# Kernel tuning notes

Measured on AMD Instinct MI355X. Metric: run time of the kernel, lower is better.

The kernel has to match this reference:

```python
import jax, jax.numpy as jnp
import numpy as np

D = 256  # atom_feature_dim
LN_EPS = 1e-5
NEG_SLOPE = 0.01  # LeakyReLU default


def setup_inputs() -> dict:
    key = jax.random.key(0)
    ks = jax.random.split(key, 8)
    B, N, L = 16, 256, 1024
    inv = 1.0 / np.sqrt(D)
    return {
        "mol_atom_feature": jax.random.normal(ks[0], (B, N, D), jnp.float32),
        "atom_feature": jax.random.normal(ks[1], (B, L, D), jnp.float32),
        "mol_atom_attend_mask": jnp.ones((B, L), jnp.float32),
        "mol_atom_softmax_mask": jnp.zeros((B, L), jnp.float32),
        # nn.Linear(D, D) params (weight stored [out, in] torch-style; we use x @ W.T form via einsum)
        "W_mol": jax.random.uniform(ks[2], (D, D), jnp.float32, -inv, inv),
        "b_mol": jnp.zeros((D,), jnp.float32),
        "W_nb": jax.random.uniform(ks[3], (D, D), jnp.float32, -inv, inv),
        "b_nb": jnp.zeros((D,), jnp.float32),
        # nn.Linear(2D, 1): weight [2D], bias scalar
        "align_w": jax.random.uniform(ks[4], (2 * D,), jnp.float32, -1.0 / np.sqrt(2 * D), 1.0 / np.sqrt(2 * D)),
        "align_b": jnp.zeros((), jnp.float32),
        "ln_gamma": jnp.ones((D,), jnp.float32),
        "ln_beta": jnp.zeros((D,), jnp.float32),
    }


def reference(mol_atom_feature, atom_feature, mol_atom_attend_mask, mol_atom_softmax_mask,
              W_mol, b_mol, W_nb, b_nb, align_w, align_b, ln_gamma, ln_beta):
    # Linear transforms (dropout is identity in eval)
    x = jnp.einsum('bnd,ed->bne', mol_atom_feature, W_mol) + b_mol   # [B,N,D]
    a = jnp.einsum('bld,ed->ble', atom_feature, W_nb) + b_nb        # [B,L,D]

    # GAT align: Linear over concat([x_i, a_j]) is separable:
    # score[b,n,l] = x[b,n]@w1 + a[b,l]@w2 + b
    w1, w2 = align_w[:D], align_w[D:]
    score = (x @ w1)[:, :, None] + (a @ w2)[:, None, :] + align_b   # [B,N,L]
    score = jax.nn.leaky_relu(score, NEG_SLOPE)

    # additive softmax mask over atom axis, then masked softmax + attend mask
    score = score + mol_atom_softmax_mask[:, None, :]
    attn = jax.nn.softmax(score, axis=-1)
    attn = attn * mol_atom_attend_mask[:, None, :]

    # weighted aggregation of transformed atom features
    ctx = jnp.einsum('bnl,bld->bnd', attn, a)                        # [B,N,D]

    # LayerNorm
    mu = jnp.mean(ctx, axis=-1, keepdims=True)
    var = jnp.var(ctx, axis=-1, keepdims=True)
    out = (ctx - mu) * jax.lax.rsqrt(var + LN_EPS) * ln_gamma + ln_beta
    return out
```

## Files before the change

kernel.cpp:

```cpp
#include <hip/hip_runtime.h>
#include <hip/hip_bf16.h>
#include <math.h>

#define BB 16
#define NN 256
#define LL 1024
#define DD 256

constexpr float LN_EPS = 1e-5f;
constexpr float NEG_SLOPE = 0.01f;

typedef __attribute__((ext_vector_type(8))) short short8;
typedef __attribute__((ext_vector_type(4))) float f32x4;
typedef __attribute__((ext_vector_type(4))) int i32x4;

static __device__ __forceinline__ unsigned cvtpk(float lo, float hi) {
  __hip_bfloat162 h = __float22bfloat162_rn(make_float2(lo, hi));
  union { __hip_bfloat162 h; unsigned u; } v; v.h = h;
  return v.u;
}
static __device__ __forceinline__ short8 pack8(float4 f0, float4 f1) {
  union { i32x4 i; short8 s; } v;
  v.i.x = cvtpk(f0.x, f0.y);
  v.i.y = cvtpk(f0.z, f0.w);
  v.i.z = cvtpk(f1.x, f1.y);
  v.i.w = cvtpk(f1.z, f1.w);
  return v.s;
}
static __device__ __forceinline__ unsigned short f2bf(float f) {
  union { float f; unsigned u; } v; v.f = f;
  unsigned r = v.u + 0x7FFFu + ((v.u >> 16) & 1u);
  return (unsigned short)(r >> 16);
}

__global__ __launch_bounds__(512) void agemm_kernel(
    const float* __restrict__ atom, const float* __restrict__ W_nb,
    const float* __restrict__ b_nb, const float* __restrict__ W_mol,
    const float* __restrict__ b_mol, const float* __restrict__ align_w,
    const float* __restrict__ align_b, unsigned short* __restrict__ aT,
    float* __restrict__ s2g, float* __restrict__ v1c) {
  __shared__ char atile[64 * 256 * 2];
  __shared__ unsigned short sAT[256 * 68];
  __shared__ float vp[32][16];
  __shared__ float s2p[8][66];

  int t = threadIdx.x;
  int w = t >> 6, lane = t & 63;
  int i = blockIdx.x;
  int x = i & 7, k = i >> 3;
  int b = x + 8 * (k >> 4);
  int l0 = (k & 15) * 64;
  int lo16 = lane & 15, g = lane >> 4;

  {
    int r = t >> 3, dseg = (t & 7) * 32;
    const float* src = atom + (size_t)(b * LL + l0 + r) * DD + dseg;
    #pragma unroll
    for (int q = 0; q < 4; ++q) {
      float4 f0 = *(const float4*)(src + q * 8);
      float4 f1 = *(const float4*)(src + q * 8 + 4);
      int byte = ((r * 256 + dseg + q * 8) * 2) ^ ((r & 7) << 4);
      *(short8*)(atile + byte) = pack8(f0, f1);
    }
  }

  if (i < 16) {
    int d0 = i * 16;
    int dl = t & 15, eseg = t >> 4;
    float acc = 0.f;
    #pragma unroll
    for (int q = 0; q < 8; ++q) {
      int e = eseg * 8 + q;
      acc += align_w[e] * W_mol[e * DD + d0 + dl];
    }
    vp[eseg][dl] = acc;
    __syncthreads();
    if (t < 16) {
      float s = 0.f;
      #pragma unroll
      for (int q = 0; q < 32; ++q) s += vp[q][t];
      v1c[d0 + t] = s;
    }
    if (i == 0 && w == 1) {
      float s = b_mol[lane] * align_w[lane] +
                b_mol[lane + 64] * align_w[lane + 64] +
                b_mol[lane + 128] * align_w[lane + 128] +
                b_mol[lane + 192] * align_w[lane + 192];
      #pragma unroll
      for (int off = 32; off > 0; off >>= 1) s += __shfl_xor(s, off, 64);
      if (lane == 0) v1c[256] = s + align_b[0];
    }
  }
  __syncthreads();

  f32x4 acc[2][4];
  #pragma unroll
  for (int m = 0; m < 2; ++m)
    #pragma unroll
    for (int n = 0; n < 4; ++n) acc[m][n] = f32x4{0.f, 0.f, 0.f, 0.f};

  const float* Ap = W_nb + (size_t)(w * 32 + lo16) * DD + g * 8;

  #pragma unroll 2
  for (int kk = 0; kk < 8; ++kk) {
    short8 af[2];
    #pragma unroll
    for (int m = 0; m < 2; ++m) {
      float4 f0 = *(const float4*)(Ap + m * 16 * DD + kk * 32);
      float4 f1 = *(const float4*)(Ap + m * 16 * DD + kk * 32 + 4);
      af[m] = pack8(f0, f1);
    }
    short8 bf[4];
    #pragma unroll
    for (int n = 0; n < 4; ++n) {
      int l = n * 16 + lo16;
      int byte = ((l * 256 + kk * 32 + g * 8) * 2) ^ ((l & 7) << 4);
      bf[n] = *(const short8*)(atile + byte);
    }
    #pragma unroll
    for (int m = 0; m < 2; ++m)
      #pragma unroll
      for (int n = 0; n < 4; ++n)
        acc[m][n] = __builtin_amdgcn_mfma_f32_16x16x32_bf16(af[m], bf[n],
                                                            acc[m][n], 0, 0, 0);
  }

  {
    float4 bias[2], w2r[2];
    #pragma unroll
    for (int m = 0; m < 2; ++m) {
      bias[m] = *(const float4*)&b_nb[w * 32 + m * 16 + g * 4];
      w2r[m] = *(const float4*)&align_w[DD + w * 32 + m * 16 + g * 4];
    }
    float p[4] = {0.f, 0.f, 0.f, 0.f};
    #pragma unroll
    for (int m = 0; m < 2; ++m) {
      #pragma unroll
      for (int n = 0; n < 4; ++n) {
        int l = n * 16 + lo16;
        #pragma unroll
        for (int jj = 0; jj < 4; ++jj) {
          float v = acc[m][n][jj] + ((const float*)&bias[m])[jj];
          sAT[(w * 32 + m * 16 + g * 4 + jj) * 68 + l] = f2bf(v);
          p[n] += ((const float*)&w2r[m])[jj] * v;
        }
      }
    }
    #pragma unroll
    for (int n = 0; n < 4; ++n) {
      p[n] += __shfl_xor(p[n], 16, 64);
      p[n] += __shfl_xor(p[n], 32, 64);
    }
    if (g == 0) {
      #pragma unroll
      for (int n = 0; n < 4; ++n) s2p[w][n * 16 + lo16] = p[n];
    }
  }
  __syncthreads();

  if (t < 64) {
    float s = 0.f;
    #pragma unroll
    for (int q = 0; q < 8; ++q) s += s2p[q][t];
    s2g[b * LL + l0 + t] = s;
  }
  unsigned short* dst = aT + (size_t)b * DD * LL + l0;
  #pragma unroll
  for (int idx = t; idx < 4096; idx += 512) {
    int e = idx >> 4, ch = idx & 15;
    ushort4 v = *(const ushort4*)&sAT[e * 68 + ch * 4];
    *(ushort4*)(dst + (size_t)e * LL + ch * 4) = v;
  }
}

__global__ __launch_bounds__(512) void attn_kernel(
    const unsigned short* __restrict__ aT, const float* __restrict__ mol,
    const float* __restrict__ v1c, const float* __restrict__ s2,
    const float* __restrict__ amask, const float* __restrict__ smask,
    const float* __restrict__ gamma, const float* __restrict__ beta,
    float* __restrict__ out) {
  __shared__ unsigned short sattn[16 * 1024];
  __shared__ float ctxp[2][16][DD];
  __shared__ float v1s[256];
  __shared__ float s1s[16];
  __shared__ float mu_s[16], rs_s[16];
  int i = blockIdx.x;
  int x = i & 7, k = i >> 3;
  int b = x + 8 * (k >> 4);
  int n0 = (k & 15) * 16;
  int t = threadIdx.x, w = t >> 6, lane = t & 63;

  float c0 = v1c[256];
  if (t < 256) v1s[t] = v1c[t];
  __syncthreads();

  {
    int r = t >> 5, off = (t & 31) * 8;
    const float* mr = mol + (size_t)(b * NN + n0 + r) * DD + off;
    float s = 0.f;
    #pragma unroll
    for (int q = 0; q < 2; ++q) {
      float4 f = *(const float4*)(mr + q * 4);
      s += f.x * v1s[off + q * 4] + f.y * v1s[off + q * 4 + 1] +
           f.z * v1s[off + q * 4 + 2] + f.w * v1s[off + q * 4 + 3];
    }
    s += __shfl_xor(s, 1, 64);
    s += __shfl_xor(s, 2, 64);
    s += __shfl_xor(s, 4, 64);
    s += __shfl_xor(s, 8, 64);
    s += __shfl_xor(s, 16, 64);
    if ((t & 31) == 0) s1s[r] = s + c0;
  }
  __syncthreads();

  {
    float s2v[16], amv[16], smv[16];
    #pragma unroll
    for (int q = 0; q < 16; ++q) {
      int l = lane + 64 * q;
      s2v[q] = s2[b * LL + l];
      amv[q] = amask[b * LL + l];
      smv[q] = smask[b * LL + l];
    }
    #pragma unroll
    for (int rr = 0; rr < 2; ++rr) {
      int r = w * 2 + rr;
      float s1v = s1s[r];
      float p[16];
      float mx = -INFINITY;
      #pragma unroll
      for (int q = 0; q < 16; ++q) {
        float sc = s1v + s2v[q];
        sc = sc > 0.f ? sc : NEG_SLOPE * sc;
        sc += smv[q];
        p[q] = sc;
        mx = fmaxf(mx, sc);
      }
      #pragma unroll
      for (int off = 32; off > 0; off >>= 1) mx = fmaxf(mx, __shfl_xor(mx, off, 64));
      float sum = 0.f;
      #pragma unroll
      for (int q = 0; q < 16; ++q) {
        p[q] = __expf(p[q] - mx);
        sum += p[q];
      }
      #pragma unroll
      for (int off = 32; off > 0; off >>= 1) sum += __shfl_xor(sum, off, 64);
      float inv = 1.f / sum;
      #pragma unroll
      for (int q = 0; q < 16; ++q) {
        unsigned short bv = f2bf(p[q] * amv[q] * inv);
        int l = lane + 64 * q;
        int byte = ((r * 1024 + l) * 2) ^ ((r & 7) << 4);
        *(unsigned short*)((char*)sattn + byte) = bv;
      }
    }
  }
  __syncthreads();

  int lo16 = lane & 15, g = lane >> 4;
  {
    int e0 = (w & 3) * 64, lh = w >> 2;
    f32x4 acc[4];
    #pragma unroll
    for (int n = 0; n < 4; ++n) acc[n] = f32x4{0.f, 0.f, 0.f, 0.f};
    const unsigned short* Bp =
        aT + (size_t)b * DD * LL + (size_t)(e0 + lo16) * LL + lh * 512 + g * 8;
    #pragma unroll 4
    for (int kk = 0; kk < 16; ++kk) {
      short8 afr = *(const short8*)((const char*)sattn +
          (((lo16 * 1024 + lh * 512 + kk * 32 + g * 8) * 2) ^ ((lo16 & 7) << 4)));
      #pragma unroll
      for (int n = 0; n < 4; ++n) {
        short8 bfr = *(const short8*)(Bp + (size_t)n * 16 * LL + kk * 32);
        acc[n] = __builtin_amdgcn_mfma_f32_16x16x32_bf16(afr, bfr, acc[n], 0, 0, 0);
      }
    }
    #pragma unroll
    for (int n = 0; n < 4; ++n)
      #pragma unroll
      for (int jj = 0; jj < 4; ++jj)
        ctxp[lh][g * 4 + jj][e0 + n * 16 + lo16] = acc[n][jj];
  }
  __syncthreads();

  #pragma unroll
  for (int rr = 0; rr < 2; ++rr) {
    int r = w * 2 + rr;
    float s = 0.f, sq = 0.f;
    #pragma unroll
    for (int jj = 0; jj < 4; ++jj) {
      int cc = lane + 64 * jj;
      float v = ctxp[0][r][cc] + ctxp[1][r][cc];
      s += v;
      sq += v * v;
    }
    #pragma unroll
    for (int off = 32; off > 0; off >>= 1) {
      s += __shfl_xor(s, off, 64);
      sq += __shfl_xor(sq, off, 64);
    }
    if (lane == 0) {
      float mu = s * (1.f / 256.f);
      float var = sq * (1.f / 256.f) - mu * mu;
      mu_s[r] = mu;
      rs_s[r] = rsqrtf(var + LN_EPS);
    }
  }
  __syncthreads();

  #pragma unroll
  for (int q = 0; q < 8; ++q) {
    int idx = t + 512 * q;
    int r = idx >> 8, d = idx & 255;
    float v = ctxp[0][r][d] + ctxp[1][r][d];
    out[(size_t)(b * NN + n0 + r) * DD + d] =
        (v - mu_s[r]) * rs_s[r] * gamma[d] + beta[d];
  }
}

extern "C" void kernel_launch(void* const* d_in, const int* in_sizes, int n_in,
                              void* d_out, int out_size, void* d_ws, size_t ws_size,
                              hipStream_t stream) {
  const float* mol     = (const float*)d_in[0];
  const float* atom    = (const float*)d_in[1];
  const float* amask   = (const float*)d_in[2];
  const float* smask   = (const float*)d_in[3];
  const float* W_mol   = (const float*)d_in[4];
  const float* b_mol   = (const float*)d_in[5];
  const float* W_nb    = (const float*)d_in[6];
  const float* b_nb    = (const float*)d_in[7];
  const float* align_w = (const float*)d_in[8];
  const float* align_b = (const float*)d_in[9];
  const float* gamma   = (const float*)d_in[10];
  const float* beta    = (const float*)d_in[11];
  float* outp = (float*)d_out;

  char* wsb = (char*)d_ws;
  unsigned short* aT = (unsigned short*)wsb;
  float* s2g = (float*)(wsb + 8388608);
  float* v1c = s2g + BB * LL;

  agemm_kernel<<<256, 512, 0, stream>>>(atom, W_nb, b_nb, W_mol, b_mol,
                                        align_w, align_b, aT, s2g, v1c);
  attn_kernel<<<256, 512, 0, stream>>>(aT, mol, v1c, s2g, amask, smask,
                                       gamma, beta, outp);
}
```

Baseline: 39.30 us.

## Fuse projection and attention kernels with per-batch atomic counter handoff

Merges the two launches into one 512-block grid. The first 256 blocks compute the atom projection and signal completion per batch through an atomic counter. The remaining blocks each recompute the W_mol·w1 vector locally and spin-wait on that counter before running the attention. This removes a kernel launch gap and lets mol-side work overlap the projection, at the cost of an extra memset, redundant v1 computation in every block, and a deadlock risk if consumer blocks become resident before all producers. Shared memory is unioned across the two phases so that more blocks can be resident at once.

```diff
diff --git a/kernel.cpp b/kernel.cpp
--- a/kernel.cpp
+++ b/kernel.cpp
@@ -33,289 +33,294 @@
   return (unsigned short)(r >> 16);
 }
 
-__global__ __launch_bounds__(512) void agemm_kernel(
-    const float* __restrict__ atom, const float* __restrict__ W_nb,
-    const float* __restrict__ b_nb, const float* __restrict__ W_mol,
-    const float* __restrict__ b_mol, const float* __restrict__ align_w,
-    const float* __restrict__ align_b, unsigned short* __restrict__ aT,
-    float* __restrict__ s2g, float* __restrict__ v1c) {
-  __shared__ char atile[64 * 256 * 2];
-  __shared__ unsigned short sAT[256 * 68];
-  __shared__ float vp[32][16];
-  __shared__ float s2p[8][66];
-
-  int t = threadIdx.x;
-  int w = t >> 6, lane = t & 63;
-  int i = blockIdx.x;
-  int x = i & 7, k = i >> 3;
-  int b = x + 8 * (k >> 4);
-  int l0 = (k & 15) * 64;
+struct P1 {
+  char atile[64 * 256 * 2];
+  unsigned short sAT[256 * 68];
+  float s2p[8][66];
+};
+struct P2 {
+  unsigned short sattn[16 * 1024];
+  float ctxp[2][16][DD];
+  float vp2[2][256];
+};
+
+__global__ __launch_bounds__(512, 4) void fused_kernel(
+    const float* __restrict__ mol, const float* __restrict__ atom,
+    const float* __restrict__ amask, const float* __restrict__ smask,
+    const float* __restrict__ W_mol, const float* __restrict__ b_mol,
+    const float* __restrict__ W_nb, const float* __restrict__ b_nb,
+    const float* __restrict__ align_w, const float* __restrict__ align_b,
+    const float* __restrict__ gamma, const float* __restrict__ beta,
+    unsigned short* __restrict__ aT, float* __restrict__ s2g,
+    unsigned int* __restrict__ cnt, float* __restrict__ out) {
+  __shared__ union { P1 p1; P2 p2; } sh;
+  __shared__ float v1s[256];
+  __shared__ float s1s[16], mu_s[16], rs_s[16];
+  __shared__ float c0s;
+
+  int t = threadIdx.x, w = t >> 6, lane = t & 63;
   int lo16 = lane & 15, g = lane >> 4;
 
-  {
-    int r = t >> 3, dseg = (t & 7) * 32;
-    const float* src = atom + (size_t)(b * LL + l0 + r) * DD + dseg;
+  if (blockIdx.x < 256) {
+    int i = blockIdx.x;
+    int x = i & 7, k = i >> 3;
+    int b = x + 8 * (k >> 4);
+    int l0 = (k & 15) * 64;
+
+    {
+      int r = t >> 3, dseg = (t & 7) * 32;
+      const float* src = atom + (size_t)(b * LL + l0 + r) * DD + dseg;
+      #pragma unroll
+      for (int q = 0; q < 4; ++q) {
+        float4 f0 = *(const float4*)(src + q * 8);
+        float4 f1 = *(const float4*)(src + q * 8 + 4);
+        int byte = ((r * 256 + dseg + q * 8) * 2) ^ ((r & 7) << 4);
+        *(short8*)(sh.p1.atile + byte) = pack8(f0, f1);
+      }
+    }
+    __syncthreads();
+
+    f32x4 acc[2][4];
     #pragma unroll
-    for (int q = 0; q < 4; ++q) {
-      float4 f0 = *(const float4*)(src + q * 8);
-      float4 f1 = *(const float4*)(src + q * 8 + 4);
-      int byte = ((r * 256 + dseg + q * 8) * 2) ^ ((r & 7) << 4);
-      *(short8*)(atile + byte) = pack8(f0, f1);
-    }
-  }
-
-  if (i < 16) {
-    int d0 = i * 16;
-    int dl = t & 15, eseg = t >> 4;
-    float acc = 0.f;
+    for (int m = 0; m < 2; ++m)
+      #pragma unroll
+      for (int n = 0; n < 4; ++n) acc[m][n] = f32x4{0.f, 0.f, 0.f, 0.f};
+
+    const float* Ap = W_nb + (size_t)(w * 32 + lo16) * DD + g * 8;
+    #pragma unroll 2
+    for (int kk = 0; kk < 8; ++kk) {
+      short8 af[2];
+      #pragma unroll
+      for (int m = 0; m < 2; ++m) {
+        float4 f0 = *(const float4*)(Ap + m * 16 * DD + kk * 32);
+        float4 f1 = *(const float4*)(Ap + m * 16 * DD + kk * 32 + 4);
+        af[m] = pack8(f0, f1);
+      }
+      short8 bf[4];
+      #pragma unroll
+      for (int n = 0; n < 4; ++n) {
+        int l = n * 16 + lo16;
+        int byte = ((l * 256 + kk * 32 + g * 8) * 2) ^ ((l & 7) << 4);
+        bf[n] = *(const short8*)(sh.p1.atile + byte);
+      }
+      #pragma unroll
+      for (int m = 0; m < 2; ++m)
+        #pragma unroll
+        for (int n = 0; n < 4; ++n)
+          acc[m][n] = __builtin_amdgcn_mfma_f32_16x16x32_bf16(af[m], bf[n],
+                                                              acc[m][n], 0, 0, 0);
+    }
+
+    {
+      float4 bias[2], w2r[2];
+      #pragma unroll
+      for (int m = 0; m < 2; ++m) {
+        bias[m] = *(const float4*)&b_nb[w * 32 + m * 16 + g * 4];
+        w2r[m] = *(const float4*)&align_w[DD + w * 32 + m * 16 + g * 4];
+      }
+      float p[4] = {0.f, 0.f, 0.f, 0.f};
+      #pragma unroll
+      for (int m = 0; m < 2; ++m) {
+        #pragma unroll
+        for (int n = 0; n < 4; ++n) {
+          int l = n * 16 + lo16;
+          #pragma unroll
+          for (int jj = 0; jj < 4; ++jj) {
+            float v = acc[m][n][jj] + ((const float*)&bias[m])[jj];
+            sh.p1.sAT[(w * 32 + m * 16 + g * 4 + jj) * 68 + l] = f2bf(v);
+            p[n] += ((const float*)&w2r[m])[jj] * v;
+          }
+        }
+      }
+      #pragma unroll
+      for (int n = 0; n < 4; ++n) {
+        p[n] += __shfl_xor(p[n], 16, 64);
+        p[n] += __shfl_xor(p[n], 32, 64);
+      }
+      if (g == 0) {
+        #pragma unroll
+        for (int n = 0; n < 4; ++n) sh.p1.s2p[w][n * 16 + lo16] = p[n];
+      }
+    }
+    __syncthreads();
+
+    if (t < 64) {
+      float s = 0.f;
+      #pragma unroll
+      for (int q = 0; q < 8; ++q) s += sh.p1.s2p[q][t];
+      s2g[b * LL + l0 + t] = s;
+    }
+    unsigned short* dst = aT + (size_t)b * DD * LL + l0;
     #pragma unroll
-    for (int q = 0; q < 8; ++q) {
-      int e = eseg * 8 + q;
-      acc += align_w[e] * W_mol[e * DD + d0 + dl];
-    }
-    vp[eseg][dl] = acc;
-    __syncthreads();
-    if (t < 16) {
-      float s = 0.f;
-      #pragma unroll
-      for (int q = 0; q < 32; ++q) s += vp[q][t];
-      v1c[d0 + t] = s;
-    }
-    if (i == 0 && w == 1) {
+    for (int idx = t; idx < 4096; idx += 512) {
+      int e = idx >> 4, ch = idx & 15;
+      ushort4 v = *(const ushort4*)&sh.p1.sAT[e * 68 + ch * 4];
+      *(ushort4*)(dst + (size_t)e * LL + ch * 4) = v;
+    }
+    __syncthreads();
+
+    if (t == 0) {
+      __hip_atomic_fetch_add(&cnt[b], 1u, __ATOMIC_RELEASE,
+                             __HIP_MEMORY_SCOPE_AGENT);
+    }
+  } else {
+    int j = blockIdx.x - 256;
+    int x = j & 7, k = j >> 3;
+    int b = x + 8 * (k >> 4);
+    int n0 = (k & 15) * 16;
+
+    {
+      int d = t & 255, eh = t >> 8;
+      float acc = 0.f;
+      #pragma unroll 8
+      for (int e = eh * 128; e < eh * 128 + 128; ++e)
+        acc += align_w[e] * W_mol[e * DD + d];
+      sh.p2.vp2[eh][d] = acc;
+    }
+    if (w == 7) {
       float s = b_mol[lane] * align_w[lane] +
                 b_mol[lane + 64] * align_w[lane + 64] +
                 b_mol[lane + 128] * align_w[lane + 128] +
                 b_mol[lane + 192] * align_w[lane + 192];
       #pragma unroll
       for (int off = 32; off > 0; off >>= 1) s += __shfl_xor(s, off, 64);
-      if (lane == 0) v1c[256] = s + align_b[0];
-    }
-  }
-  __syncthreads();
-
-  f32x4 acc[2][4];
-  #pragma unroll
-  for (int m = 0; m < 2; ++m)
-    #pragma unroll
-    for (int n = 0; n < 4; ++n) acc[m][n] = f32x4{0.f, 0.f, 0.f, 0.f};
-
-  const float* Ap = W_nb + (size_t)(w * 32 + lo16) * DD + g * 8;
-
-  #pragma unroll 2
-  for (int kk = 0; kk < 8; ++kk) {
-    short8 af[2];
-    #pragma unroll
-    for (int m = 0; m < 2; ++m) {
-      float4 f0 = *(const float4*)(Ap + m * 16 * DD + kk * 32);
-      float4 f1 = *(const float4*)(Ap + m * 16 * DD + kk * 32 + 4);
-      af[m] = pack8(f0, f1);
-    }
-    short8 bf[4];
-    #pragma unroll
-    for (int n = 0; n < 4; ++n) {
-      int l = n * 16 + lo16;
-      int byte = ((l * 256 + kk * 32 + g * 8) * 2) ^ ((l & 7) << 4);
-      bf[n] = *(const short8*)(atile + byte);
-    }
-    #pragma unroll
-    for (int m = 0; m < 2; ++m)
+      if (lane == 0) c0s = s + align_b[0];
+    }
+    __syncthreads();
+    if (t < 256) v1s[t] = sh.p2.vp2[0][t] + sh.p2.vp2[1][t];
+    __syncthreads();
+
+    {
+      int r = t >> 5, off = (t & 31) * 8;
+      const float* mr = mol + (size_t)(b * NN + n0 + r) * DD + off;
+      float s = 0.f;
+      #pragma unroll
+      for (int q = 0; q < 2; ++q) {
+        float4 f = *(const float4*)(mr + q * 4);
+        s += f.x * v1s[off + q * 4] + f.y * v1s[off + q * 4 + 1] +
+             f.z * v1s[off + q * 4 + 2] + f.w * v1s[off + q * 4 + 3];
+      }
+      s += __shfl_xor(s, 1, 64);
+      s += __shfl_xor(s, 2, 64);
+      s += __shfl_xor(s, 4, 64);
+      s += __shfl_xor(s, 8, 64);
+      s += __shfl_xor(s, 16, 64);
+      if ((t & 31) == 0) s1s[r] = s + c0s;
+    }
+    __syncthreads();
+
+    if (t == 0) {
+      while (__hip_atomic_load(&cnt[b], __ATOMIC_ACQUIRE,
+                               __HIP_MEMORY_SCOPE_AGENT) < 16u) {
+        __builtin_amdgcn_s_sleep(8);
+      }
+      __threadfence();
+    }
+    __syncthreads();
+
+    {
+      float s2v[16], amv[16], smv[16];
+      #pragma unroll
+      for (int q = 0; q < 16; ++q) {
+        int l = lane + 64 * q;
+        s2v[q] = s2g[b * LL + l];
+        amv[q] = amask[b * LL + l];
+        smv[q] = smask[b * LL + l];
+      }
+      #pragma unroll
+      for (int rr = 0; rr < 2; ++rr) {
+        int r = w * 2 + rr;
+        float s1v = s1s[r];
+        float p[16];
+        float mx = -INFINITY;
+        #pragma unroll
+        for (int q = 0; q < 16; ++q) {
+          float sc = s1v + s2v[q];
+          sc = sc > 0.f ? sc : NEG_SLOPE * sc;
+          sc += smv[q];
+          p[q] = sc;
+          mx = fmaxf(mx, sc);
+        }
+        #pragma unroll
+        for (int off = 32; off > 0; off >>= 1) mx = fmaxf(mx, __shfl_xor(mx, off, 64));
+        float sum = 0.f;
+        #pragma unroll
+        for (int q = 0; q < 16; ++q) {
+          p[q] = __expf(p[q] - mx);
+          sum += p[q];
+        }
+        #pragma unroll
+        for (int off = 32; off > 0; off >>= 1) sum += __shfl_xor(sum, off, 64);
+        float inv = 1.f / sum;
+        #pragma unroll
+        for (int q = 0; q < 16; ++q) {
+          unsigned short bv = f2bf(p[q] * amv[q] * inv);
+          int l = lane + 64 * q;
+          int byte = ((r * 1024 + l) * 2) ^ ((r & 7) << 4);
+          *(unsigned short*)((char*)sh.p2.sattn + byte) = bv;
+        }
+      }
+    }
+    __syncthreads();
+
+    {
+      int e0 = (w & 3) * 64, lh = w >> 2;
+      f32x4 acc[4];
+      #pragma unroll
+      for (int n = 0; n < 4; ++n) acc[n] = f32x4{0.f, 0.f, 0.f, 0.f};
+      const unsigned short* Bp =
+          aT + (size_t)b * DD * LL + (size_t)(e0 + lo16) * LL + lh * 512 + g * 8;
+      #pragma unroll 4
+      for (int kk = 0; kk < 16; ++kk) {
+        short8 afr = *(const short8*)((const char*)sh.p2.sattn +
+            (((lo16 * 1024 + lh * 512 + kk * 32 + g * 8) * 2) ^ ((lo16 & 7) << 4)));
+        #pragma unroll
+        for (int n = 0; n < 4; ++n) {
+          short8 bfr = *(const short8*)(Bp + (size_t)n * 16 * LL + kk * 32);
+          acc[n] = __builtin_amdgcn_mfma_f32_16x16x32_bf16(afr, bfr, acc[n], 0, 0, 0);
+        }
+      }
       #pragma unroll
       for (int n = 0; n < 4; ++n)
-        acc[m][n] = __builtin_amdgcn_mfma_f32_16x16x32_bf16(af[m], bf[n],
-                                                            acc[m][n], 0, 0, 0);
-  }
-
-  {
-    float4 bias[2], w2r[2];
-    #pragma unroll
-    for (int m = 0; m < 2; ++m) {
-      bias[m] = *(const float4*)&b_nb[w * 32 + m * 16 + g * 4];
-      w2r[m] = *(const float4*)&align_w[DD + w * 32 + m * 16 + g * 4];
-    }
-    float p[4] = {0.f, 0.f, 0.f, 0.f};
-    #pragma unroll
-    for (int m = 0; m < 2; ++m) {
-      #pragma unroll
-      for (int n = 0; n < 4; ++n) {
-        int l = n * 16 + lo16;
-        #pragma unroll
-        for (int jj = 0; jj < 4; ++jj) {
-          float v = acc[m][n][jj] + ((const float*)&bias[m])[jj];
-          sAT[(w * 32 + m * 16 + g * 4 + jj) * 68 + l] = f2bf(v);
-          p[n] += ((const float*)&w2r[m])[jj] * v;
-        }
-      }
-    }
-    #pragma unroll
-    for (int n = 0; n < 4; ++n) {
-      p[n] += __shfl_xor(p[n], 16, 64);
-      p[n] += __shfl_xor(p[n], 32, 64);
-    }
-    if (g == 0) {
-      #pragma unroll
-      for (int n = 0; n < 4; ++n) s2p[w][n * 16 + lo16] = p[n];
-    }
-  }
-  __syncthreads();
-
-  if (t < 64) {
-    float s = 0.f;
-    #pragma unroll
-    for (int q = 0; q < 8; ++q) s += s2p[q][t];
-    s2g[b * LL + l0 + t] = s;
-  }
-  unsigned short* dst = aT + (size_t)b * DD * LL + l0;
-  #pragma unroll
-  for (int idx = t; idx < 4096; idx += 512) {
-    int e = idx >> 4, ch = idx & 15;
-    ushort4 v = *(const ushort4*)&sAT[e * 68 + ch * 4];
-    *(ushort4*)(dst + (size_t)e * LL + ch * 4) = v;
-  }
-}
-
-__global__ __launch_bounds__(512) void attn_kernel(
-    const unsigned short* __restrict__ aT, const float* __restrict__ mol,
-    const float* __restrict__ v1c, const float* __restrict__ s2,
-    const float* __restrict__ amask, const float* __restrict__ smask,
-    const float* __restrict__ gamma, const float* __restrict__ beta,
-    float* __restrict__ out) {
-  __shared__ unsigned short sattn[16 * 1024];
-  __shared__ float ctxp[2][16][DD];
-  __shared__ float v1s[256];
-  __shared__ float s1s[16];
-  __shared__ float mu_s[16], rs_s[16];
-  int i = blockIdx.x;
-  int x = i & 7, k = i >> 3;
-  int b = x + 8 * (k >> 4);
-  int n0 = (k & 15) * 16;
-  int t = threadIdx.x, w = t >> 6, lane = t & 63;
-
-  float c0 = v1c[256];
-  if (t < 256) v1s[t] = v1c[t];
-  __syncthreads();
-
-  {
-    int r = t >> 5, off = (t & 31) * 8;
-    const float* mr = mol + (size_t)(b * NN + n0 + r) * DD + off;
-    float s = 0.f;
-    #pragma unroll
-    for (int q = 0; q < 2; ++q) {
-      float4 f = *(const float4*)(mr + q * 4);
-      s += f.x * v1s[off + q * 4] + f.y * v1s[off + q * 4 + 1] +
-           f.z * v1s[off + q * 4 + 2] + f.w * v1s[off + q * 4 + 3];
-    }
-    s += __shfl_xor(s, 1, 64);
-    s += __shfl_xor(s, 2, 64);
-    s += __shfl_xor(s, 4, 64);
-    s += __shfl_xor(s, 8, 64);
-    s += __shfl_xor(s, 16, 64);
-    if ((t & 31) == 0) s1s[r] = s + c0;
-  }
-  __syncthreads();
-
-  {
-    float s2v[16], amv[16], smv[16];
-    #pragma unroll
-    for (int q = 0; q < 16; ++q) {
-      int l = lane + 64 * q;
-      s2v[q] = s2[b * LL + l];
-      amv[q] = amask[b * LL + l];
-      smv[q] = smask[b * LL + l];
-    }
+        #pragma unroll
+        for (int jj = 0; jj < 4; ++jj)
+          sh.p2.ctxp[lh][g * 4 + jj][e0 + n * 16 + lo16] = acc[n][jj];
+    }
+    __syncthreads();
+
     #pragma unroll
     for (int rr = 0; rr < 2; ++rr) {
       int r = w * 2 + rr;
-      float s1v = s1s[r];
-      float p[16];
-      float mx = -INFINITY;
-      #pragma unroll
-      for (int q = 0; q < 16; ++q) {
-        float sc = s1v + s2v[q];
-        sc = sc > 0.f ? sc : NEG_SLOPE * sc;
-        sc += smv[q];
-        p[q] = sc;
-        mx = fmaxf(mx, sc);
-      }
-      #pragma unroll
-      for (int off = 32; off > 0; off >>= 1) mx = fmaxf(mx, __shfl_xor(mx, off, 64));
-      float sum = 0.f;
-      #pragma unroll
-      for (int q = 0; q < 16; ++q) {
-        p[q] = __expf(p[q] - mx);
-        sum += p[q];
-      }
-      #pragma unroll
-      for (int off = 32; off > 0; off >>= 1) sum += __shfl_xor(sum, off, 64);
-      float inv = 1.f / sum;
-      #pragma unroll
-      for (int q = 0; q < 16; ++q) {
-        unsigned short bv = f2bf(p[q] * amv[q] * inv);
-        int l = lane + 64 * q;
-        int byte = ((r * 1024 + l) * 2) ^ ((r & 7) << 4);
-        *(unsigned short*)((char*)sattn + byte) = bv;
-      }
-    }
-  }
-  __syncthreads();
-
-  int lo16 = lane & 15, g = lane >> 4;
-  {
-    int e0 = (w & 3) * 64, lh = w >> 2;
-    f32x4 acc[4];
+      float s = 0.f, sq = 0.f;
+      #pragma unroll
+      for (int jj = 0; jj < 4; ++jj) {
+        int cc = lane + 64 * jj;
+        float v = sh.p2.ctxp[0][r][cc] + sh.p2.ctxp[1][r][cc];
+        s += v;
+        sq += v * v;
+      }
+      #pragma unroll
+      for (int off = 32; off > 0; off >>= 1) {
+        s += __shfl_xor(s, off, 64);
+        sq += __shfl_xor(sq, off, 64);
+      }
+      if (lane == 0) {
+        float mu = s * (1.f / 256.f);
+        float var = sq * (1.f / 256.f) - mu * mu;
+        mu_s[r] = mu;
+        rs_s[r] = rsqrtf(var + LN_EPS);
+      }
+    }
+    __syncthreads();
+
     #pragma unroll
-    for (int n = 0; n < 4; ++n) acc[n] = f32x4{0.f, 0.f, 0.f, 0.f};
-    const unsigned short* Bp =
-        aT + (size_t)b * DD * LL + (size_t)(e0 + lo16) * LL + lh * 512 + g * 8;
-    #pragma unroll 4
-    for (int kk = 0; kk < 16; ++kk) {
-      short8 afr = *(const short8*)((const char*)sattn +
-          (((lo16 * 1024 + lh * 512 + kk * 32 + g * 8) * 2) ^ ((lo16 & 7) << 4)));
-      #pragma unroll
-      for (int n = 0; n < 4; ++n) {
-        short8 bfr = *(const short8*)(Bp + (size_t)n * 16 * LL + kk * 32);
-        acc[n] = __builtin_amdgcn_mfma_f32_16x16x32_bf16(afr, bfr, acc[n], 0, 0, 0);
-      }
-    }
-    #pragma unroll
-    for (int n = 0; n < 4; ++n)
-      #pragma unroll
-      for (int jj = 0; jj < 4; ++jj)
-        ctxp[lh][g * 4 + jj][e0 + n * 16 + lo16] = acc[n][jj];
-  }
-  __syncthreads();
-
-  #pragma unroll
-  for (int rr = 0; rr < 2; ++rr) {
-    int r = w * 2 + rr;
-    float s = 0.f, sq = 0.f;
-    #pragma unroll
-    for (int jj = 0; jj < 4; ++jj) {
-      int cc = lane + 64 * jj;
-      float v = ctxp[0][r][cc] + ctxp[1][r][cc];
-      s += v;
-      sq += v * v;
-    }
-    #pragma unroll
-    for (int off = 32; off > 0; off >>= 1) {
-      s += __shfl_xor(s, off, 64);
-      sq += __shfl_xor(sq, off, 64);
-    }
-    if (lane == 0) {
-      float mu = s * (1.f / 256.f);
-      float var = sq * (1.f / 256.f) - mu * mu;
-      mu_s[r] = mu;
-      rs_s[r] = rsqrtf(var + LN_EPS);
-    }
-  }
-  __syncthreads();
-
-  #pragma unroll
-  for (int q = 0; q < 8; ++q) {
-    int idx = t + 512 * q;
-    int r = idx >> 8, d = idx & 255;
-    float v = ctxp[0][r][d] + ctxp[1][r][d];
-    out[(size_t)(b * NN + n0 + r) * DD + d] =
-        (v - mu_s[r]) * rs_s[r] * gamma[d] + beta[d];
+    for (int q = 0; q < 8; ++q) {
+      int idx = t + 512 * q;
+      int r = idx >> 8, d = idx & 255;
+      float v = sh.p2.ctxp[0][r][d] + sh.p2.ctxp[1][r][d];
+      out[(size_t)(b * NN + n0 + r) * DD + d] =
+          (v - mu_s[r]) * rs_s[r] * gamma[d] + beta[d];
+    }
   }
 }
 
@@ -339,10 +344,10 @@
   char* wsb = (char*)d_ws;
   unsigned short* aT = (unsigned short*)wsb;
   float* s2g = (float*)(wsb + 8388608);
-  float* v1c = s2g + BB * LL;
-
-  agemm_kernel<<<256, 512, 0, stream>>>(atom, W_nb, b_nb, W_mol, b_mol,
-                                        align_w, align_b, aT, s2g, v1c);
-  attn_kernel<<<256, 512, 0, stream>>>(aT, mol, v1c, s2g, amask, smask,
-                                       gamma, beta, outp);
-}
+  unsigned int* cnt = (unsigned int*)(wsb + 8388608 + 65536);
+
+  hipMemsetAsync(cnt, 0, 16 * sizeof(unsigned int), stream);
+  fused_kernel<<<512, 512, 0, stream>>>(mol, atom, amask, smask, W_mol, b_mol,
+                                        W_nb, b_nb, align_w, align_b, gamma,
+                                        beta, aT, s2g, cnt, outp);
+}
```

Result: slower. 56.41 us (+43.5%).
